# Kernel tuning notes

Hardware: AMD Instinct MI355X
Metric: run time of the kernel (lower is better)

The kernel has to match this reference:

```python
import jax, jax.numpy as jnp
import numpy as np

B = 262144
N_MAX = 4
N_EXPERTS = sum(n * n for n in range(1, N_MAX + 1))  # 30
# offset of expert block for each n (experts within n indexed by l*l + l + m)
OFFSETS = np.cumsum([0] + [n * n for n in range(1, N_MAX)])  # [0,1,5,14]


def _expert_id(n, l, m):
    off = jnp.asarray(OFFSETS, dtype=jnp.int32)
    return off[n - 1] + l * l + l + m  # (B,) int


def setup_inputs() -> dict:
    key = jax.random.key(0)
    ks = jax.random.split(key, 12)
    x = jax.random.normal(ks[0], (B, 3), dtype=jnp.float32)
    # valid coupled quantum numbers: 1<=n<=4, 0<=l<n, -l<=m<=l
    n = jax.random.randint(ks[1], (B,), 1, N_MAX + 1)
    ul = jax.random.uniform(ks[2], (B,))
    l = jnp.floor(ul * n.astype(jnp.float32)).astype(jnp.int32)
    l = jnp.clip(l, 0, n - 1)
    um = jax.random.uniform(ks[3], (B,))
    m = jnp.floor(um * (2 * l + 1).astype(jnp.float32)).astype(jnp.int32) - l
    m = jnp.clip(m, -l, l)
    s = 0.1
    W0 = jax.random.normal(ks[4], (3, 128), dtype=jnp.float32) * s
    b0 = jnp.zeros((128,), dtype=jnp.float32)
    W1 = jax.random.normal(ks[5], (128, 64), dtype=jnp.float32) * s
    b1 = jnp.zeros((64,), dtype=jnp.float32)
    Wa = jax.random.normal(ks[6], (N_EXPERTS, 64, 32), dtype=jnp.float32) * s
    ba = jax.random.normal(ks[7], (N_EXPERTS, 32), dtype=jnp.float32) * s
    Wb = jax.random.normal(ks[8], (N_EXPERTS, 32, 2), dtype=jnp.float32) * s
    bb = jax.random.normal(ks[9], (N_EXPERTS, 2), dtype=jnp.float32) * s
    return {"x": x, "n": n.astype(jnp.int32), "l": l, "m": m,
            "W0": W0, "b0": b0, "W1": W1, "b1": b1,
            "Wa": Wa, "ba": ba, "Wb": Wb, "bb": bb}


def reference(x, n, l, m, W0, b0, W1, b1, Wa, ba, Wb, bb):
    eid = _expert_id(n, l, m)  # (B,)
    # shared trunk (dropout is identity in eval mode)
    h = jnp.tanh(x @ W0 + b0)          # (B,128)
    h = jnp.tanh(h @ W1 + b1)          # (B,64)
    # per-sample expert dispatch via irregular gather of tiny MLP weights
    g = jnp.tanh(jnp.einsum('bd,bdh->bh', h, Wa[eid]) + ba[eid])  # (B,32)
    psi = jnp.einsum('bh,bho->bo', g, Wb[eid]) + bb[eid]          # (B,2)
    norm = jnp.sqrt(jnp.sum(psi * psi, axis=1, keepdims=True) + 1e-6)
    return psi / norm
```

## Files before the change

kernel.cpp:

```cpp
#include <hip/hip_runtime.h>
#include <math.h>


#define THREADS 256
#define NE 30
#define HB 128
#define MAXBLK 1056
#define SA 259
#define SG 36

typedef short bf16x8 __attribute__((ext_vector_type(8)));
typedef float f32x4 __attribute__((ext_vector_type(4)));

__device__ __forceinline__ int expert_id(int nn, int ll, int mm) {
    return ((nn - 1) * nn * (2 * nn - 1)) / 6 + ll * ll + ll + mm;
}

__device__ __forceinline__ float fast_tanh(float v) {
    float e = __builtin_exp2f(v * 2.885390082f);
    return fmaf(-2.0f, __builtin_amdgcn_rcpf(e + 1.0f), 1.0f);
}

__device__ __forceinline__ unsigned int f2b(float f) {
    unsigned int u = __float_as_uint(f);
    return (u + 0x7fffu + ((u >> 16) & 1u)) >> 16;
}
__device__ __forceinline__ float b2f(unsigned int b) {
    return __uint_as_float(b << 16);
}
__device__ __forceinline__ unsigned int packsplit(float v) {
    unsigned int hb = f2b(v);
    unsigned int lb = f2b(v - b2f(hb));
    return (lb << 16) | hb;
}

union U8 { unsigned int u[4]; bf16x8 v; };
__device__ __forceinline__ void unpack8(const unsigned int* w, bf16x8& hi, bf16x8& lo) {
    U8 H, L;
#pragma unroll
    for (int i = 0; i < 4; ++i) {
        H.u[i] = (w[2 * i + 1] << 16) | (w[2 * i] & 0xffffu);
        L.u[i] = (w[2 * i + 1] & 0xffff0000u) | (w[2 * i] >> 16);
    }
    hi = H.v; lo = L.v;
}

__global__ void hist_pack_kernel(const int* __restrict__ nq, const int* __restrict__ lq,
                                 const int* __restrict__ mq, int* __restrict__ hist,
                                 int* __restrict__ eids,
                                 const float* __restrict__ W1, unsigned int* __restrict__ W1pk,
                                 const float* __restrict__ Wa, unsigned int* __restrict__ Wapk,
                                 int B) {
    const int tid = threadIdx.x;
    const int bx = blockIdx.x;
    if (bx < HB) {
        __shared__ int h[NE];
        if (tid < NE) h[tid] = 0;
        __syncthreads();
        const int per = B / HB, base = bx * per;
        for (int i = tid; i < per; i += blockDim.x) {
            const int e = expert_id(nq[base + i], lq[base + i], mq[base + i]);
            eids[base + i] = e;
            atomicAdd(&h[e], 1);
        }
        __syncthreads();
        if (tid < NE) hist[bx * NE + tid] = h[tid];
    } else if (bx < HB + 4) {
        const int seg = bx - HB;
        for (int i = seg * 2048 + tid; i < (seg + 1) * 2048; i += blockDim.x) {
            const int n = i >> 7, k = i & 127;
            W1pk[i] = packsplit(W1[k * 64 + n]);
        }
    } else {
        const int e = bx - HB - 4;
        for (int i = tid; i < 2048; i += blockDim.x) {
            const int hh = i >> 6, d = i & 63;
            Wapk[e * 2048 + i] = packsplit(Wa[e * 2048 + d * 32 + hh]);
        }
    }
}

__global__ void plan_kernel(const int* __restrict__ hist, int* __restrict__ base,
                            int4* __restrict__ btab) {
    __shared__ int sh[HB * NE];
    __shared__ int tot[NE], off[NE], sstart[NE], snb[NE];
    const int tid = threadIdx.x;
    for (int i = tid; i < HB * NE; i += blockDim.x) sh[i] = hist[i];
    __syncthreads();
    if (tid < NE) {
        int s = 0;
        for (int b = 0; b < HB; ++b) s += sh[b * NE + tid];
        tot[tid] = s;
    }
    __syncthreads();
    if (tid == 0) {
        int acc = 0, slot = 0;
        for (int e = 0; e < NE; ++e) {
            off[e] = acc;
            int nb = (tot[e] + THREADS - 1) / THREADS;
            sstart[e] = slot; snb[e] = nb;
            slot += nb; acc += tot[e];
        }
    }
    __syncthreads();
    if (tid < NE) {
        int acc = off[tid];
        for (int b = 0; b < HB; ++b) { base[b * NE + tid] = acc; acc += sh[b * NE + tid]; }
    }
    for (int e = 0; e < NE; ++e) {
        for (int j = tid; j < snb[e]; j += blockDim.x) {
            int4 bt;
            bt.x = e;
            bt.y = off[e] + j * THREADS;
            bt.z = min(THREADS, tot[e] - j * THREADS);
            bt.w = 0;
            btab[sstart[e] + j] = bt;
        }
    }
    __syncthreads();
    const int total = sstart[NE - 1] + snb[NE - 1];
    for (int s = total + tid; s < MAXBLK; s += blockDim.x) {
        int4 bt; bt.x = 0; bt.y = 0; bt.z = 0; bt.w = 0;
        btab[s] = bt;
    }
}

__global__ void scatter_kernel(const int* __restrict__ eids, const int* __restrict__ base,
                               int* __restrict__ perm, int B) {
    __shared__ int cnt[NE];
    const int tid = threadIdx.x;
    if (tid < NE) cnt[tid] = base[blockIdx.x * NE + tid];
    __syncthreads();
    const int per = B / gridDim.x;
    const int blk = blockIdx.x * per;
    for (int i = tid; i < per; i += blockDim.x) {
        const int idx = blk + i;
        const int dst = atomicAdd(&cnt[eids[idx]], 1);
        perm[dst] = idx;
    }
}

__global__ __launch_bounds__(THREADS, 3) void wfc_kernel(
    const float* __restrict__ x, const int* __restrict__ perm,
    const int4* __restrict__ btab,
    const float* __restrict__ W0, const float* __restrict__ b0,
    const unsigned int* __restrict__ W1pk, const float* __restrict__ b1,
    const unsigned int* __restrict__ Wapk, const float* __restrict__ ba,
    const float* __restrict__ Wb, const float* __restrict__ bb,
    float* __restrict__ out)
{
    __shared__ unsigned int sbuf[9216];

    const int4 bt = btab[blockIdx.x];
    if (bt.z == 0) return;
    const int eid = __builtin_amdgcn_readfirstlane(bt.x);
    const int tid = threadIdx.x;
    const bool valid = tid < bt.z;
    const int idx = perm[bt.y + (valid ? tid : 0)];

    const int lane = tid & 63;
    const int wv   = tid >> 6;
    const int qd   = lane >> 4;
    const int l16  = lane & 15;

    const float x0 = x[idx * 3 + 0];
    const float x1 = x[idx * 3 + 1];
    const float x2 = x[idx * 3 + 2];

    f32x4 acc[4][4];
#pragma unroll
    for (int nt = 0; nt < 4; ++nt) {
        const float bv = b1[nt * 16 + l16];
#pragma unroll
        for (int mt = 0; mt < 4; ++mt) {
            f32x4 c; c[0] = bv; c[1] = bv; c[2] = bv; c[3] = bv;
            acc[mt][nt] = c;
        }
    }

    for (int c = 0; c < 4; ++c) {
        if (c) __syncthreads();
#pragma unroll
        for (int kk = 0; kk < 32; ++kk) {
            const int k = c * 32 + kk;
            const float pre = fmaf(x0, W0[k], fmaf(x1, W0[128 + k], fmaf(x2, W0[256 + k], b0[k])));
            sbuf[kk * SA + tid] = packsplit(fast_tanh(pre));
        }
        __syncthreads();

        bf16x8 Bhi[4], Blo[4];
#pragma unroll
        for (int nt = 0; nt < 4; ++nt) {
            const uint4* p = (const uint4*)(W1pk + (nt * 16 + l16) * 128 + c * 32 + qd * 8);
            uint4 u0 = p[0], u1 = p[1];
            unsigned int w[8] = {u0.x, u0.y, u0.z, u0.w, u1.x, u1.y, u1.z, u1.w};
            unpack8(w, Bhi[nt], Blo[nt]);
        }
#pragma unroll
        for (int mt = 0; mt < 4; ++mt) {
            unsigned int a[8];
            const int mrow = wv * 64 + mt * 16 + l16;
#pragma unroll
            for (int j = 0; j < 8; ++j) a[j] = sbuf[(qd * 8 + j) * SA + mrow];
            bf16x8 Ahi, Alo;
            unpack8(a, Ahi, Alo);
#pragma unroll
            for (int nt = 0; nt < 4; ++nt) {
                acc[mt][nt] = __builtin_amdgcn_mfma_f32_16x16x32_bf16(Ahi, Bhi[nt], acc[mt][nt], 0, 0, 0);
                acc[mt][nt] = __builtin_amdgcn_mfma_f32_16x16x32_bf16(Ahi, Blo[nt], acc[mt][nt], 0, 0, 0);
                acc[mt][nt] = __builtin_amdgcn_mfma_f32_16x16x32_bf16(Alo, Bhi[nt], acc[mt][nt], 0, 0, 0);
            }
        }
    }

    f32x4 acc2[4][2];
#pragma unroll
    for (int nt2 = 0; nt2 < 2; ++nt2) {
        const float bv = ba[(eid << 5) + nt2 * 16 + l16];
#pragma unroll
        for (int mt = 0; mt < 4; ++mt) {
            f32x4 c; c[0] = bv; c[1] = bv; c[2] = bv; c[3] = bv;
            acc2[mt][nt2] = c;
        }
    }

    for (int c2 = 0; c2 < 2; ++c2) {
        __syncthreads();
#pragma unroll
        for (int mt = 0; mt < 4; ++mt) {
#pragma unroll
            for (int ntl = 0; ntl < 2; ++ntl) {
#pragma unroll
                for (int r = 0; r < 4; ++r) {
                    const float h2 = fast_tanh(acc[mt][c2 * 2 + ntl][r]);
                    const int dl  = ntl * 16 + l16;
                    const int row = wv * 64 + mt * 16 + qd * 4 + r;
                    sbuf[dl * SA + row] = packsplit(h2);
                }
            }
        }
        __syncthreads();

        bf16x8 B2hi[2], B2lo[2];
#pragma unroll
        for (int nt2 = 0; nt2 < 2; ++nt2) {
            const uint4* p = (const uint4*)(Wapk + eid * 2048 + (nt2 * 16 + l16) * 64 + c2 * 32 + qd * 8);
            uint4 u0 = p[0], u1 = p[1];
            unsigned int w[8] = {u0.x, u0.y, u0.z, u0.w, u1.x, u1.y, u1.z, u1.w};
            unpack8(w, B2hi[nt2], B2lo[nt2]);
        }
#pragma unroll
        for (int mt = 0; mt < 4; ++mt) {
            unsigned int a[8];
            const int mrow = wv * 64 + mt * 16 + l16;
#pragma unroll
            for (int j = 0; j < 8; ++j) a[j] = sbuf[(qd * 8 + j) * SA + mrow];
            bf16x8 Ahi, Alo;
            unpack8(a, Ahi, Alo);
#pragma unroll
            for (int nt2 = 0; nt2 < 2; ++nt2) {
                acc2[mt][nt2] = __builtin_amdgcn_mfma_f32_16x16x32_bf16(Ahi, B2hi[nt2], acc2[mt][nt2], 0, 0, 0);
                acc2[mt][nt2] = __builtin_amdgcn_mfma_f32_16x16x32_bf16(Ahi, B2lo[nt2], acc2[mt][nt2], 0, 0, 0);
                acc2[mt][nt2] = __builtin_amdgcn_mfma_f32_16x16x32_bf16(Alo, B2hi[nt2], acc2[mt][nt2], 0, 0, 0);
            }
        }
    }

    __syncthreads();
    float* g2 = (float*)sbuf;
#pragma unroll
    for (int mt = 0; mt < 4; ++mt) {
#pragma unroll
        for (int nt2 = 0; nt2 < 2; ++nt2) {
#pragma unroll
            for (int r = 0; r < 4; ++r) {
                const int row = wv * 64 + mt * 16 + qd * 4 + r;
                g2[row * SG + nt2 * 16 + l16] = fast_tanh(acc2[mt][nt2][r]);
            }
        }
    }
    __syncthreads();

    float gv[32];
    {
        const float4* grow = (const float4*)(g2 + tid * SG);
#pragma unroll
        for (int i = 0; i < 8; ++i) {
            float4 v = grow[i];
            gv[4 * i + 0] = v.x; gv[4 * i + 1] = v.y;
            gv[4 * i + 2] = v.z; gv[4 * i + 3] = v.w;
        }
    }

    const float* __restrict__ wbe = Wb + (eid << 6);
    float p0 = bb[2 * eid], p1 = bb[2 * eid + 1];
#pragma unroll
    for (int h = 0; h < 32; ++h) {
        p0 = fmaf(gv[h], wbe[2 * h + 0], p0);
        p1 = fmaf(gv[h], wbe[2 * h + 1], p1);
    }

    const float s = fmaf(p0, p0, fmaf(p1, p1, 1e-6f));
    const float inv = 1.0f / sqrtf(s);
    if (valid) {
        float2 o; o.x = p0 * inv; o.y = p1 * inv;
        ((float2*)out)[idx] = o;
    }
}

extern "C" void kernel_launch(void* const* d_in, const int* in_sizes, int n_in,
                              void* d_out, int out_size, void* d_ws, size_t ws_size,
                              hipStream_t stream) {
    const float* x  = (const float*)d_in[0];
    const int*   n  = (const int*)d_in[1];
    const int*   l  = (const int*)d_in[2];
    const int*   m  = (const int*)d_in[3];
    const float* W0 = (const float*)d_in[4];
    const float* b0 = (const float*)d_in[5];
    const float* W1 = (const float*)d_in[6];
    const float* b1 = (const float*)d_in[7];
    const float* Wa = (const float*)d_in[8];
    const float* ba = (const float*)d_in[9];
    const float* Wb = (const float*)d_in[10];
    const float* bb = (const float*)d_in[11];
    float* out = (float*)d_out;

    const int B = in_sizes[1];

    int*          perm = (int*)d_ws;
    int*          eids = perm + B;
    int4*         btab = (int4*)(eids + B);
    int*          hist = (int*)(btab + MAXBLK);
    int*          base = hist + HB * NE;
    unsigned int* W1pk = (unsigned int*)(base + HB * NE);
    unsigned int* Wapk = W1pk + 64 * 128;

    hist_pack_kernel<<<HB + 4 + NE, 256, 0, stream>>>(n, l, m, hist, eids, W1, W1pk, Wa, Wapk, B);
    plan_kernel<<<1, 256, 0, stream>>>(hist, base, btab);
    scatter_kernel<<<HB, 256, 0, stream>>>(eids, base, perm, B);
    wfc_kernel<<<MAXBLK, THREADS, 0, stream>>>(
        x, perm, btab, W0, b0, W1pk, b1, Wapk, ba, Wb, bb, out);
}
```

Baseline: 153.8 us.

## Drop plan kernel, use atomic block offsets and fragment-ordered bf16 weights

The single-block plan kernel is removed. Each histogram block now reserves its per-expert base with a global atomicAdd on the expert totals, scatter computes expert starts from those totals, and the main kernel finds its expert segment by a small loop over the totals. The hi/lo bf16 weight halves are also pre-laid out in MFMA fragment order, so the main kernel loads bf16x8 vectors directly and skips the unpack shuffles. This cuts one serial launch and per-block unpacking, at the cost of a memset and nondeterministic (but still valid) permutation order.

```diff
diff --git a/kernel.cpp b/kernel.cpp
--- a/kernel.cpp
+++ b/kernel.cpp
@@ -46,10 +46,13 @@
 }
 
 __global__ void hist_pack_kernel(const int* __restrict__ nq, const int* __restrict__ lq,
-                                 const int* __restrict__ mq, int* __restrict__ hist,
-                                 int* __restrict__ eids,
-                                 const float* __restrict__ W1, unsigned int* __restrict__ W1pk,
-                                 const float* __restrict__ Wa, unsigned int* __restrict__ Wapk,
+                                 const int* __restrict__ mq,
+                                 int* __restrict__ eids, int* __restrict__ etot,
+                                 int* __restrict__ bbase,
+                                 const float* __restrict__ W1,
+                                 unsigned short* __restrict__ W1fh, unsigned short* __restrict__ W1fl,
+                                 const float* __restrict__ Wa,
+                                 unsigned short* __restrict__ Wafh, unsigned short* __restrict__ Wafl,
                                  int B) {
     const int tid = threadIdx.x;
     const int bx = blockIdx.x;
@@ -64,99 +67,85 @@
             atomicAdd(&h[e], 1);
         }
         __syncthreads();
-        if (tid < NE) hist[bx * NE + tid] = h[tid];
-    } else if (bx < HB + 4) {
-        const int seg = bx - HB;
-        for (int i = seg * 2048 + tid; i < (seg + 1) * 2048; i += blockDim.x) {
-            const int n = i >> 7, k = i & 127;
-            W1pk[i] = packsplit(W1[k * 64 + n]);
+        if (tid < NE) bbase[bx * NE + tid] = atomicAdd(&etot[tid], h[tid]);
+    } else if (bx == HB) {
+        for (int i = tid; i < 8192; i += blockDim.x) {
+            const int j = i & 7, l16 = (i >> 3) & 15, qd = (i >> 7) & 3;
+            const int nt = (i >> 9) & 3, c = i >> 11;
+            const int k = c * 32 + qd * 8 + j, n = nt * 16 + l16;
+            const float w = W1[k * 64 + n];
+            const unsigned int hb = f2b(w);
+            W1fh[i] = (unsigned short)hb;
+            W1fl[i] = (unsigned short)f2b(w - b2f(hb));
         }
     } else {
-        const int e = bx - HB - 4;
+        const int e = bx - HB - 1;
         for (int i = tid; i < 2048; i += blockDim.x) {
-            const int hh = i >> 6, d = i & 63;
-            Wapk[e * 2048 + i] = packsplit(Wa[e * 2048 + d * 32 + hh]);
-        }
-    }
-}
-
-__global__ void plan_kernel(const int* __restrict__ hist, int* __restrict__ base,
-                            int4* __restrict__ btab) {
-    __shared__ int sh[HB * NE];
-    __shared__ int tot[NE], off[NE], sstart[NE], snb[NE];
+            const int j = i & 7, l16 = (i >> 3) & 15, qd = (i >> 7) & 3;
+            const int nt2 = (i >> 9) & 1, c2 = (i >> 10) & 1;
+            const int d = c2 * 32 + qd * 8 + j, hh = nt2 * 16 + l16;
+            const float w = Wa[e * 2048 + d * 32 + hh];
+            const unsigned int hb = f2b(w);
+            Wafh[e * 2048 + i] = (unsigned short)hb;
+            Wafl[e * 2048 + i] = (unsigned short)f2b(w - b2f(hb));
+        }
+    }
+}
+
+__global__ void scatter_kernel(const int* __restrict__ eids, const int* __restrict__ etot,
+                               const int* __restrict__ bbase, int* __restrict__ perm, int B) {
+    __shared__ int lcnt[NE], esrt[NE], bb[NE];
     const int tid = threadIdx.x;
-    for (int i = tid; i < HB * NE; i += blockDim.x) sh[i] = hist[i];
-    __syncthreads();
-    if (tid < NE) {
-        int s = 0;
-        for (int b = 0; b < HB; ++b) s += sh[b * NE + tid];
-        tot[tid] = s;
-    }
-    __syncthreads();
+    if (tid < NE) { lcnt[tid] = 0; bb[tid] = bbase[blockIdx.x * NE + tid]; }
     if (tid == 0) {
-        int acc = 0, slot = 0;
-        for (int e = 0; e < NE; ++e) {
-            off[e] = acc;
-            int nb = (tot[e] + THREADS - 1) / THREADS;
-            sstart[e] = slot; snb[e] = nb;
-            slot += nb; acc += tot[e];
-        }
-    }
-    __syncthreads();
-    if (tid < NE) {
-        int acc = off[tid];
-        for (int b = 0; b < HB; ++b) { base[b * NE + tid] = acc; acc += sh[b * NE + tid]; }
-    }
-    for (int e = 0; e < NE; ++e) {
-        for (int j = tid; j < snb[e]; j += blockDim.x) {
-            int4 bt;
-            bt.x = e;
-            bt.y = off[e] + j * THREADS;
-            bt.z = min(THREADS, tot[e] - j * THREADS);
-            bt.w = 0;
-            btab[sstart[e] + j] = bt;
-        }
-    }
-    __syncthreads();
-    const int total = sstart[NE - 1] + snb[NE - 1];
-    for (int s = total + tid; s < MAXBLK; s += blockDim.x) {
-        int4 bt; bt.x = 0; bt.y = 0; bt.z = 0; bt.w = 0;
-        btab[s] = bt;
-    }
-}
-
-__global__ void scatter_kernel(const int* __restrict__ eids, const int* __restrict__ base,
-                               int* __restrict__ perm, int B) {
-    __shared__ int cnt[NE];
-    const int tid = threadIdx.x;
-    if (tid < NE) cnt[tid] = base[blockIdx.x * NE + tid];
+        int es = 0;
+        for (int e = 0; e < NE; ++e) { esrt[e] = es; es += etot[e]; }
+    }
     __syncthreads();
     const int per = B / gridDim.x;
     const int blk = blockIdx.x * per;
     for (int i = tid; i < per; i += blockDim.x) {
         const int idx = blk + i;
-        const int dst = atomicAdd(&cnt[eids[idx]], 1);
-        perm[dst] = idx;
+        const int e = eids[idx];
+        const int r = atomicAdd(&lcnt[e], 1);
+        perm[esrt[e] + bb[e] + r] = idx;
     }
 }
 
 __global__ __launch_bounds__(THREADS, 3) void wfc_kernel(
     const float* __restrict__ x, const int* __restrict__ perm,
-    const int4* __restrict__ btab,
+    const int* __restrict__ etot,
     const float* __restrict__ W0, const float* __restrict__ b0,
-    const unsigned int* __restrict__ W1pk, const float* __restrict__ b1,
-    const unsigned int* __restrict__ Wapk, const float* __restrict__ ba,
+    const bf16x8* __restrict__ W1fh, const bf16x8* __restrict__ W1fl,
+    const float* __restrict__ b1,
+    const bf16x8* __restrict__ Wafh, const bf16x8* __restrict__ Wafl,
+    const float* __restrict__ ba,
     const float* __restrict__ Wb, const float* __restrict__ bb,
     float* __restrict__ out)
 {
     __shared__ unsigned int sbuf[9216];
 
-    const int4 bt = btab[blockIdx.x];
-    if (bt.z == 0) return;
-    const int eid = __builtin_amdgcn_readfirstlane(bt.x);
+    int eid = -1, start = 0, cnt = 0;
+    {
+        int cum = 0, es = 0;
+#pragma unroll 1
+        for (int e = 0; e < NE; ++e) {
+            const int t = etot[e];
+            const int nb = (t + THREADS - 1) >> 8;
+            if ((int)blockIdx.x < cum + nb) {
+                const int seg = blockIdx.x - cum;
+                eid = e; start = es + seg * THREADS; cnt = min(THREADS, t - seg * THREADS);
+                break;
+            }
+            cum += nb; es += t;
+        }
+    }
+    if (eid < 0) return;
+    eid = __builtin_amdgcn_readfirstlane(eid);
+
     const int tid = threadIdx.x;
-    const bool valid = tid < bt.z;
-    const int idx = perm[bt.y + (valid ? tid : 0)];
+    const bool valid = tid < cnt;
+    const int idx = perm[start + (valid ? tid : 0)];
 
     const int lane = tid & 63;
     const int wv   = tid >> 6;
@@ -191,10 +180,9 @@
         bf16x8 Bhi[4], Blo[4];
 #pragma unroll
         for (int nt = 0; nt < 4; ++nt) {
-            const uint4* p = (const uint4*)(W1pk + (nt * 16 + l16) * 128 + c * 32 + qd * 8);
-            uint4 u0 = p[0], u1 = p[1];
-            unsigned int w[8] = {u0.x, u0.y, u0.z, u0.w, u1.x, u1.y, u1.z, u1.w};
-            unpack8(w, Bhi[nt], Blo[nt]);
+            const int rec = (c * 4 + nt) * 64 + qd * 16 + l16;
+            Bhi[nt] = W1fh[rec];
+            Blo[nt] = W1fl[rec];
         }
 #pragma unroll
         for (int mt = 0; mt < 4; ++mt) {
@@ -224,6 +212,8 @@
         }
     }
 
+    const bf16x8* __restrict__ waeh = Wafh + (eid << 8);
+    const bf16x8* __restrict__ wael = Wafl + (eid << 8);
     for (int c2 = 0; c2 < 2; ++c2) {
         __syncthreads();
 #pragma unroll
@@ -244,10 +234,9 @@
         bf16x8 B2hi[2], B2lo[2];
 #pragma unroll
         for (int nt2 = 0; nt2 < 2; ++nt2) {
-            const uint4* p = (const uint4*)(Wapk + eid * 2048 + (nt2 * 16 + l16) * 64 + c2 * 32 + qd * 8);
-            uint4 u0 = p[0], u1 = p[1];
-            unsigned int w[8] = {u0.x, u0.y, u0.z, u0.w, u1.x, u1.y, u1.z, u1.w};
-            unpack8(w, B2hi[nt2], B2lo[nt2]);
+            const int rec = (c2 * 2 + nt2) * 64 + qd * 16 + l16;
+            B2hi[nt2] = waeh[rec];
+            B2lo[nt2] = wael[rec];
         }
 #pragma unroll
         for (int mt = 0; mt < 4; ++mt) {
@@ -327,17 +316,21 @@
 
     const int B = in_sizes[1];
 
-    int*          perm = (int*)d_ws;
-    int*          eids = perm + B;
-    int4*         btab = (int4*)(eids + B);
-    int*          hist = (int*)(btab + MAXBLK);
-    int*          base = hist + HB * NE;
-    unsigned int* W1pk = (unsigned int*)(base + HB * NE);
-    unsigned int* Wapk = W1pk + 64 * 128;
-
-    hist_pack_kernel<<<HB + 4 + NE, 256, 0, stream>>>(n, l, m, hist, eids, W1, W1pk, Wa, Wapk, B);
-    plan_kernel<<<1, 256, 0, stream>>>(hist, base, btab);
-    scatter_kernel<<<HB, 256, 0, stream>>>(eids, base, perm, B);
+    int*            perm = (int*)d_ws;
+    int*            eids = perm + B;
+    int*            bbase = eids + B;
+    int*            etot  = bbase + HB * NE;
+    unsigned short* W1fh  = (unsigned short*)(etot + 32);
+    unsigned short* W1fl  = W1fh + 8192;
+    unsigned short* Wafh  = W1fl + 8192;
+    unsigned short* Wafl  = Wafh + NE * 2048;
+
+    hipMemsetAsync(etot, 0, 32 * sizeof(int), stream);
+    hist_pack_kernel<<<HB + 1 + NE, 256, 0, stream>>>(
+        n, l, m, eids, etot, bbase, W1, W1fh, W1fl, Wa, Wafh, Wafl, B);
+    scatter_kernel<<<HB, 256, 0, stream>>>(eids, etot, bbase, perm, B);
     wfc_kernel<<<MAXBLK, THREADS, 0, stream>>>(
-        x, perm, btab, W0, b0, W1pk, b1, Wapk, ba, Wb, bb, out);
-}
+        x, perm, etot, W0, b0,
+        (const bf16x8*)W1fh, (const bf16x8*)W1fl, b1,
+        (const bf16x8*)Wafh, (const bf16x8*)Wafl, ba, Wb, bb, out);
+}
```

New measurement: 146.4 us. 4.8% less time.
